# Kernel tuning notes

Measured on AMD Instinct MI355X. Metric: run time of the kernel, lower is better.

## Reference

```python
import jax, jax.numpy as jnp
import numpy as np

N, D, E = 10000, 64, 32768   # nodes, padded degree, target edges
F, H, O = 64, 256, 1         # in_channels, hidden_channels, out_channels


def _linear_init(key, fin, fout):
    kw, kb = jax.random.split(key)
    s = 1.0 / np.sqrt(fin)
    w = jax.random.uniform(kw, (fin, fout), jnp.float32, -s, s)
    b = jax.random.uniform(kb, (fout,), jnp.float32, -s, s)
    return w, b


def setup_inputs() -> dict:
    key = jax.random.key(0)
    ks = jax.random.split(key, 12)
    x = jax.random.normal(ks[0], (N, F), jnp.float32)
    adj_nbr = jax.random.randint(ks[1], (N, D), 0, N)          # padded neighbor lists
    tar_ei = jax.random.randint(ks[2], (2, E), 0, N)           # target edges
    xcn_w1, xcn_b1 = _linear_init(ks[3], F, H)
    xcn_w2, xcn_b2 = _linear_init(ks[4], H, H)
    xcn_w3, xcn_b3 = _linear_init(ks[5], H, H)
    xij_w1, xij_b1 = _linear_init(ks[6], F, H)
    xij_w2, xij_b2 = _linear_init(ks[7], H, H)
    lin_w1, lin_b1 = _linear_init(ks[8], H, H)
    lin_w2, lin_b2 = _linear_init(ks[9], H, O)
    beta = jnp.ones((1,), jnp.float32)
    return dict(x=x, adj_nbr=adj_nbr, tar_ei=tar_ei, beta=beta,
                xcn_w1=xcn_w1, xcn_b1=xcn_b1, xcn_w2=xcn_w2, xcn_b2=xcn_b2,
                xcn_w3=xcn_w3, xcn_b3=xcn_b3,
                xij_w1=xij_w1, xij_b1=xij_b1, xij_w2=xij_w2, xij_b2=xij_b2,
                lin_w1=lin_w1, lin_b1=lin_b1, lin_w2=lin_w2, lin_b2=lin_b2)


def reference(x, adj_nbr, tar_ei, beta,
              xcn_w1, xcn_b1, xcn_w2, xcn_b2, xcn_w3, xcn_b3,
              xij_w1, xij_b1, xij_w2, xij_b2,
              lin_w1, lin_b1, lin_w2, lin_b2):
    relu = jax.nn.relu
    i, j = tar_ei[0], tar_ei[1]
    # adjoverlap: common-neighbor intersection of rows i and j of the adjacency
    ni = adj_nbr[i]                                   # [E, D] neighbors of i
    nj = adj_nbr[j]                                   # [E, D] neighbors of j
    cm = (ni[:, :, None] == nj[:, None, :]).any(-1)   # [E, D] ni[a] in N(j)?
    # spmm_add(cn, x): sum features of common neighbors per target edge
    xcn = jnp.einsum('ed,edf->ef', cm.astype(x.dtype), x[ni])  # [E, F]
    # xijlin(xi * xj): Linear -> ReLU -> Linear
    xij = x[i] * x[j]
    h_ij = relu(xij @ xij_w1 + xij_b1) @ xij_w2 + xij_b2
    # xcnlin(xcn): Linear -> ReLU -> Linear -> ReLU -> Linear
    h_cn = relu(xcn @ xcn_w1 + xcn_b1)
    h_cn = relu(h_cn @ xcn_w2 + xcn_b2)
    h_cn = h_cn @ xcn_w3 + xcn_b3
    # lin(xcnlin(xcn) * beta + xij): Linear -> ReLU -> Linear
    h = relu((h_cn * beta + h_ij) @ lin_w1 + lin_b1)
    return h @ lin_w2 + lin_b2                        # [E, O]
```

## Files before the change

kernel.cpp:

```cpp
#include <hip/hip_runtime.h>

#define NNODES 10000
#define DDEG   64
#define NEDGES 32768
#define FIN    64
#define HID    256

typedef __attribute__((ext_vector_type(8))) __bf16 bf16x8;
typedef __attribute__((ext_vector_type(4))) float  f32x4;

__device__ __forceinline__ unsigned short f2bf(float f) {
    unsigned x = __float_as_uint(f);
    return (unsigned short)((x + 0x7FFFu + ((x >> 16) & 1u)) >> 16);
}
__device__ __forceinline__ float b2f(unsigned short u) {
    return __uint_as_float(((unsigned)u) << 16);
}

#define OFF_XIJ1 0
#define OFF_XIJ2 16384
#define OFF_XCN1 81920
#define OFF_XCN2 98304
#define OFF_XCN3 163840
#define OFF_LIN1 229376
#define WT_TOTAL 294912
#define NTILES   36

__host__ __device__ constexpr int tile_off(int t) {
    return t < 2  ? OFF_XIJ1 + t * 8192
         : t < 10 ? OFF_XIJ2 + (t - 2) * 8192
         : t < 12 ? OFF_XCN1 + (t - 10) * 8192
         : t < 20 ? OFF_XCN2 + (t - 12) * 8192
         : t < 28 ? OFF_XCN3 + (t - 20) * 8192
         :          OFF_LIN1 + (t - 28) * 8192;
}

__device__ __forceinline__ void gll16(const unsigned short* g, unsigned short* l) {
    __builtin_amdgcn_global_load_lds(
        (const __attribute__((address_space(1))) unsigned int*)g,
        (__attribute__((address_space(3))) unsigned int*)l, 16, 0, 0);
}
__device__ __forceinline__ void stage_tile(const unsigned short* g, unsigned short* l,
                                           int tid, int wv) {
#pragma unroll
    for (int c = 0; c < 2; ++c)
        gll16(g + c * 4096 + tid * 8, l + c * 4096 + wv * 512);
}

__global__ __launch_bounds__(256) void edge_prep_k(const float* __restrict__ x,
                                                   const int* __restrict__ adj,
                                                   const int* __restrict__ tar,
                                                   const float* __restrict__ xij_w1,
                                                   const float* __restrict__ xij_w2,
                                                   const float* __restrict__ xcn_w1,
                                                   const float* __restrict__ xcn_w2,
                                                   const float* __restrict__ xcn_w3,
                                                   const float* __restrict__ lin_w1,
                                                   unsigned short* __restrict__ WT,
                                                   unsigned short* __restrict__ xij_g,
                                                   unsigned short* __restrict__ xcn_g) {
    const int wv   = threadIdx.x >> 6;
    const int lane = threadIdx.x & 63;
    const int e    = blockIdx.x * 4 + wv;

    int i = tar[e];
    int j = tar[NEDGES + e];
    int ni = adj[i * DDEG + lane];
    int nj = adj[j * DDEG + lane];
    float xi = x[i * FIN + lane];
    float xj = x[j * FIN + lane];

    bool found = false;
#pragma unroll
    for (int b = 0; b < 64; ++b)
        found |= (ni == (int)__builtin_amdgcn_readlane(nj, b));
    unsigned long long m = __ballot(found);

    float acc = 0.f;
    while (m) {
        int a = __ffsll(m) - 1;
        m &= m - 1;
        int r = (int)__builtin_amdgcn_readlane(ni, a);
        acc += x[r * FIN + lane];
    }
    int sl = lane ^ ((e & 7) << 3);
    xij_g[(size_t)e * FIN + sl] = f2bf(xi * xj);
    xcn_g[(size_t)e * FIN + sl] = f2bf(acc);

    if (blockIdx.x < WT_TOTAL / 256) {
        int idx = blockIdx.x * 256 + threadIdx.x;
        const float* src;
        int r;
        if (idx < OFF_XIJ2)      { r = idx - OFF_XIJ1; src = xij_w1; }
        else if (idx < OFF_XCN1) { r = idx - OFF_XIJ2; src = xij_w2; }
        else if (idx < OFF_XCN2) { r = idx - OFF_XCN1; src = xcn_w1; }
        else if (idx < OFF_XCN3) { r = idx - OFF_XCN2; src = xcn_w2; }
        else if (idx < OFF_LIN1) { r = idx - OFF_XCN3; src = xcn_w3; }
        else                     { r = idx - OFF_LIN1; src = lin_w1; }
        int kb  = r >> 13;
        int n   = (r & 8191) >> 5;
        int klo = r & 31;
        WT[idx] = f2bf(src[(kb * 32 + klo) * HID + n]);
    }
}

template <int T0, int NT, int LDA>
__device__ __forceinline__ void run_phase(const unsigned short* As,
                                          unsigned short* ring,
                                          const unsigned short* __restrict__ WT,
                                          int lr, int lg, int col0, int r0,
                                          int tid, int wv, f32x4 acc[4][4]) {
#pragma unroll
    for (int m = 0; m < 4; ++m)
#pragma unroll
        for (int n = 0; n < 4; ++n) acc[m][n] = (f32x4){0.f, 0.f, 0.f, 0.f};
    const int sw = (lr & 7) << 3;
#pragma unroll
    for (int s = 0; s < NT; ++s) {
        const int t = T0 + s;
        if (t < NTILES - 1)
            asm volatile("s_waitcnt vmcnt(2) lgkmcnt(0)" ::: "memory");
        else
            asm volatile("s_waitcnt vmcnt(0) lgkmcnt(0)" ::: "memory");
        __builtin_amdgcn_s_barrier();
        if (t + 2 < NTILES)
            stage_tile(WT + tile_off(t + 2), ring + ((t + 2) % 3) * 8192, tid, wv);
        const unsigned short* cur = ring + (t % 3) * 8192;
        bf16x8 a[4], b[4];
#pragma unroll
        for (int n = 0; n < 4; ++n)
            b[n] = *reinterpret_cast<const bf16x8*>(&cur[(col0 + n * 16 + lr) * 32 + 8 * lg]);
#pragma unroll
        for (int m = 0; m < 4; ++m)
            a[m] = *reinterpret_cast<const bf16x8*>(
                &As[(r0 + m * 16 + lr) * LDA + ((s * 32 + 8 * lg) ^ sw)]);
        __builtin_amdgcn_s_setprio(1);
#pragma unroll
        for (int m = 0; m < 4; ++m)
#pragma unroll
            for (int n = 0; n < 4; ++n)
                acc[m][n] = __builtin_amdgcn_mfma_f32_16x16x32_bf16(a[m], b[n], acc[m][n], 0, 0, 0);
        __builtin_amdgcn_s_setprio(0);
    }
}

__global__ __launch_bounds__(512, 1) void mlp_k(const unsigned short* __restrict__ xij_g,
                                                const unsigned short* __restrict__ xcn_g,
                                                const unsigned short* __restrict__ WT,
                                                const float* __restrict__ xij_b1,
                                                const float* __restrict__ xij_b2,
                                                const float* __restrict__ xcn_b1,
                                                const float* __restrict__ xcn_b2,
                                                const float* __restrict__ xcn_b3,
                                                const float* __restrict__ lin_b1,
                                                const float* __restrict__ lin_w2,
                                                const float* __restrict__ lin_b2,
                                                const float* __restrict__ beta,
                                                float* __restrict__ out) {
    __shared__ unsigned short sXij[128 * 64];
    __shared__ unsigned short sXcn[128 * 64];
    __shared__ unsigned short sH[128 * 256];
    __shared__ unsigned short sB[3 * 8192];

    const int tid  = threadIdx.x;
    const int wv   = tid >> 6;
    const int lane = tid & 63;
    const int lr   = lane & 15;
    const int lg   = lane >> 4;
    const int r0   = (wv >> 2) * 64;
    const int col0 = (wv & 3) * 64;
    const int row0 = blockIdx.x * 128;

    stage_tile(xij_g + (size_t)row0 * FIN, sXij, tid, wv);
    stage_tile(xcn_g + (size_t)row0 * FIN, sXcn, tid, wv);
    stage_tile(WT + tile_off(0), sB, tid, wv);
    stage_tile(WT + tile_off(1), sB + 8192, tid, wv);
    const float betaf = beta[0];

    f32x4 acc[4][4];
    float bl[4];

    run_phase<0, 2, 64>(sXij, sB, WT, lr, lg, col0, r0, tid, wv, acc);
#pragma unroll
    for (int n = 0; n < 4; ++n) bl[n] = xij_b1[col0 + n * 16 + lr];
#pragma unroll
    for (int m = 0; m < 4; ++m)
#pragma unroll
        for (int n = 0; n < 4; ++n)
#pragma unroll
            for (int i = 0; i < 4; ++i) {
                int row = r0 + m * 16 + 4 * lg + i;
                int col = col0 + n * 16 + lr;
                sH[row * HID + (col ^ ((row & 7) << 3))] = f2bf(fmaxf(acc[m][n][i] + bl[n], 0.f));
            }

    run_phase<2, 8, 256>(sH, sB, WT, lr, lg, col0, r0, tid, wv, acc);
#pragma unroll
    for (int n = 0; n < 4; ++n) bl[n] = xij_b2[col0 + n * 16 + lr];
    unsigned hij_lo[4][4], hij_hi[4][4];
#pragma unroll
    for (int m = 0; m < 4; ++m)
#pragma unroll
        for (int n = 0; n < 4; ++n) {
            hij_lo[m][n] = ((unsigned)f2bf(acc[m][n][1] + bl[n]) << 16) | f2bf(acc[m][n][0] + bl[n]);
            hij_hi[m][n] = ((unsigned)f2bf(acc[m][n][3] + bl[n]) << 16) | f2bf(acc[m][n][2] + bl[n]);
        }

    run_phase<10, 2, 64>(sXcn, sB, WT, lr, lg, col0, r0, tid, wv, acc);
#pragma unroll
    for (int n = 0; n < 4; ++n) bl[n] = xcn_b1[col0 + n * 16 + lr];
#pragma unroll
    for (int m = 0; m < 4; ++m)
#pragma unroll
        for (int n = 0; n < 4; ++n)
#pragma unroll
            for (int i = 0; i < 4; ++i) {
                int row = r0 + m * 16 + 4 * lg + i;
                int col = col0 + n * 16 + lr;
                sH[row * HID + (col ^ ((row & 7) << 3))] = f2bf(fmaxf(acc[m][n][i] + bl[n], 0.f));
            }

    run_phase<12, 8, 256>(sH, sB, WT, lr, lg, col0, r0, tid, wv, acc);
    asm volatile("s_waitcnt lgkmcnt(0)" ::: "memory");
    __builtin_amdgcn_s_barrier();
#pragma unroll
    for (int n = 0; n < 4; ++n) bl[n] = xcn_b2[col0 + n * 16 + lr];
#pragma unroll
    for (int m = 0; m < 4; ++m)
#pragma unroll
        for (int n = 0; n < 4; ++n)
#pragma unroll
            for (int i = 0; i < 4; ++i) {
                int row = r0 + m * 16 + 4 * lg + i;
                int col = col0 + n * 16 + lr;
                sH[row * HID + (col ^ ((row & 7) << 3))] = f2bf(fmaxf(acc[m][n][i] + bl[n], 0.f));
            }

    run_phase<20, 8, 256>(sH, sB, WT, lr, lg, col0, r0, tid, wv, acc);
    asm volatile("s_waitcnt lgkmcnt(0)" ::: "memory");
    __builtin_amdgcn_s_barrier();
#pragma unroll
    for (int n = 0; n < 4; ++n) bl[n] = xcn_b3[col0 + n * 16 + lr];
#pragma unroll
    for (int m = 0; m < 4; ++m)
#pragma unroll
        for (int n = 0; n < 4; ++n) {
            float h0 = b2f((unsigned short)(hij_lo[m][n] & 0xFFFF));
            float h1 = b2f((unsigned short)(hij_lo[m][n] >> 16));
            float h2 = b2f((unsigned short)(hij_hi[m][n] & 0xFFFF));
            float h3 = b2f((unsigned short)(hij_hi[m][n] >> 16));
            float v0 = (acc[m][n][0] + bl[n]) * betaf + h0;
            float v1 = (acc[m][n][1] + bl[n]) * betaf + h1;
            float v2 = (acc[m][n][2] + bl[n]) * betaf + h2;
            float v3 = (acc[m][n][3] + bl[n]) * betaf + h3;
            int rb = r0 + m * 16 + 4 * lg;
            int col = col0 + n * 16 + lr;
            sH[(rb + 0) * HID + (col ^ (((rb + 0) & 7) << 3))] = f2bf(v0);
            sH[(rb + 1) * HID + (col ^ (((rb + 1) & 7) << 3))] = f2bf(v1);
            sH[(rb + 2) * HID + (col ^ (((rb + 2) & 7) << 3))] = f2bf(v2);
            sH[(rb + 3) * HID + (col ^ (((rb + 3) & 7) << 3))] = f2bf(v3);
        }

    run_phase<28, 8, 256>(sH, sB, WT, lr, lg, col0, r0, tid, wv, acc);
#pragma unroll
    for (int n = 0; n < 4; ++n) bl[n] = lin_b1[col0 + n * 16 + lr];
    float w2l[4];
#pragma unroll
    for (int n = 0; n < 4; ++n) w2l[n] = lin_w2[col0 + n * 16 + lr];
    float* sRed = (float*)sXij;
#pragma unroll
    for (int m = 0; m < 4; ++m) {
        float p[4] = {0.f, 0.f, 0.f, 0.f};
#pragma unroll
        for (int n = 0; n < 4; ++n)
#pragma unroll
            for (int i = 0; i < 4; ++i)
                p[i] += fmaxf(acc[m][n][i] + bl[n], 0.f) * w2l[n];
#pragma unroll
        for (int i = 0; i < 4; ++i) {
            float s = p[i];
            s += __shfl_xor(s, 1);
            s += __shfl_xor(s, 2);
            s += __shfl_xor(s, 4);
            s += __shfl_xor(s, 8);
            if (lr == 0) sRed[(wv & 3) * 128 + r0 + m * 16 + 4 * lg + i] = s;
        }
    }
    __syncthreads();
    if (tid < 128)
        out[row0 + tid] = sRed[tid] + sRed[128 + tid] + sRed[256 + tid] + sRed[384 + tid] + lin_b2[0];
}

extern "C" void kernel_launch(void* const* d_in, const int* in_sizes, int n_in,
                              void* d_out, int out_size, void* d_ws, size_t ws_size,
                              hipStream_t stream) {
    const float* x      = (const float*)d_in[0];
    const int*   adj    = (const int*)d_in[1];
    const int*   tar    = (const int*)d_in[2];
    const float* beta   = (const float*)d_in[3];
    const float* xcn_w1 = (const float*)d_in[4];
    const float* xcn_b1 = (const float*)d_in[5];
    const float* xcn_w2 = (const float*)d_in[6];
    const float* xcn_b2 = (const float*)d_in[7];
    const float* xcn_w3 = (const float*)d_in[8];
    const float* xcn_b3 = (const float*)d_in[9];
    const float* xij_w1 = (const float*)d_in[10];
    const float* xij_b1 = (const float*)d_in[11];
    const float* xij_w2 = (const float*)d_in[12];
    const float* xij_b2 = (const float*)d_in[13];
    const float* lin_w1 = (const float*)d_in[14];
    const float* lin_b1 = (const float*)d_in[15];
    const float* lin_w2 = (const float*)d_in[16];
    const float* lin_b2 = (const float*)d_in[17];

    unsigned short* WT    = (unsigned short*)d_ws;
    unsigned short* xij_g = (unsigned short*)((char*)d_ws + 589824);
    unsigned short* xcn_g = (unsigned short*)((char*)d_ws + 4784128);

    edge_prep_k<<<NEDGES / 4, 256, 0, stream>>>(x, adj, tar,
                                                xij_w1, xij_w2, xcn_w1, xcn_w2, xcn_w3, lin_w1,
                                                WT, xij_g, xcn_g);
    mlp_k<<<NEDGES / 128, 512, 0, stream>>>(xij_g, xcn_g, WT,
                                            xij_b1, xij_b2, xcn_b1, xcn_b2, xcn_b3,
                                            lin_b1, lin_w2, lin_b2, beta, (float*)d_out);
}
```

Before: 62.60 us.

## Stage weight tiles in pairs, spill h_ij to global, share one input buffer

```diff
diff --git a/kernel.cpp b/kernel.cpp
--- a/kernel.cpp
+++ b/kernel.cpp
@@ -25,6 +25,7 @@
 #define OFF_LIN1 229376
 #define WT_TOTAL 294912
 #define NTILES   36
+#define NSS_ALL  18
 
 __host__ __device__ constexpr int tile_off(int t) {
     return t < 2  ? OFF_XIJ1 + t * 8192
@@ -45,6 +46,14 @@
 #pragma unroll
     for (int c = 0; c < 2; ++c)
         gll16(g + c * 4096 + tid * 8, l + c * 4096 + wv * 512);
+}
+__device__ __forceinline__ void stage_pair(const unsigned short* __restrict__ WT, int g,
+                                           unsigned short* ring, int tid, int wv) {
+    const unsigned short* src = WT + tile_off(2 * g);
+    unsigned short* dst = ring + ((2 * g) & 3) * 8192;
+#pragma unroll
+    for (int c = 0; c < 4; ++c)
+        gll16(src + c * 4096 + tid * 8, dst + c * 4096 + wv * 512);
 }
 
 __global__ __launch_bounds__(256) void edge_prep_k(const float* __restrict__ x,
@@ -104,10 +113,12 @@
     }
 }
 
-template <int T0, int NT, int LDA>
+template <int G0, int NSS, int LDA>
 __device__ __forceinline__ void run_phase(const unsigned short* As,
                                           unsigned short* ring,
                                           const unsigned short* __restrict__ WT,
+                                          const unsigned short* __restrict__ restage_src,
+                                          unsigned short* sX,
                                           int lr, int lg, int col0, int r0,
                                           int tid, int wv, f32x4 acc[4][4]) {
 #pragma unroll
@@ -116,37 +127,42 @@
         for (int n = 0; n < 4; ++n) acc[m][n] = (f32x4){0.f, 0.f, 0.f, 0.f};
     const int sw = (lr & 7) << 3;
 #pragma unroll
-    for (int s = 0; s < NT; ++s) {
-        const int t = T0 + s;
-        if (t < NTILES - 1)
-            asm volatile("s_waitcnt vmcnt(2) lgkmcnt(0)" ::: "memory");
-        else
-            asm volatile("s_waitcnt vmcnt(0) lgkmcnt(0)" ::: "memory");
+    for (int ss = 0; ss < NSS; ++ss) {
+        const int g = G0 + ss;
+        asm volatile("s_waitcnt vmcnt(0) lgkmcnt(0)" ::: "memory");
         __builtin_amdgcn_s_barrier();
-        if (t + 2 < NTILES)
-            stage_tile(WT + tile_off(t + 2), ring + ((t + 2) % 3) * 8192, tid, wv);
-        const unsigned short* cur = ring + (t % 3) * 8192;
-        bf16x8 a[4], b[4];
-#pragma unroll
-        for (int n = 0; n < 4; ++n)
-            b[n] = *reinterpret_cast<const bf16x8*>(&cur[(col0 + n * 16 + lr) * 32 + 8 * lg]);
-#pragma unroll
-        for (int m = 0; m < 4; ++m)
-            a[m] = *reinterpret_cast<const bf16x8*>(
-                &As[(r0 + m * 16 + lr) * LDA + ((s * 32 + 8 * lg) ^ sw)]);
-        __builtin_amdgcn_s_setprio(1);
-#pragma unroll
-        for (int m = 0; m < 4; ++m)
+        if (g + 1 < NSS_ALL)
+            stage_pair(WT, g + 1, ring, tid, wv);
+        if (restage_src && ss == 0)
+            stage_tile(restage_src, sX, tid, wv);
+#pragma unroll
+        for (int half = 0; half < 2; ++half) {
+            const int t  = 2 * g + half;
+            const int kk = (ss * 2 + half) * 32;
+            const unsigned short* cur = ring + (t & 3) * 8192;
+            bf16x8 a[4], b[4];
 #pragma unroll
             for (int n = 0; n < 4; ++n)
-                acc[m][n] = __builtin_amdgcn_mfma_f32_16x16x32_bf16(a[m], b[n], acc[m][n], 0, 0, 0);
-        __builtin_amdgcn_s_setprio(0);
+                b[n] = *reinterpret_cast<const bf16x8*>(&cur[(col0 + n * 16 + lr) * 32 + 8 * lg]);
+#pragma unroll
+            for (int m = 0; m < 4; ++m)
+                a[m] = *reinterpret_cast<const bf16x8*>(
+                    &As[(r0 + m * 16 + lr) * LDA + ((kk + 8 * lg) ^ sw)]);
+            __builtin_amdgcn_s_setprio(1);
+#pragma unroll
+            for (int m = 0; m < 4; ++m)
+#pragma unroll
+                for (int n = 0; n < 4; ++n)
+                    acc[m][n] = __builtin_amdgcn_mfma_f32_16x16x32_bf16(a[m], b[n], acc[m][n], 0, 0, 0);
+            __builtin_amdgcn_s_setprio(0);
+        }
     }
 }
 
 __global__ __launch_bounds__(512, 1) void mlp_k(const unsigned short* __restrict__ xij_g,
                                                 const unsigned short* __restrict__ xcn_g,
                                                 const unsigned short* __restrict__ WT,
+                                                unsigned* __restrict__ hij_g,
                                                 const float* __restrict__ xij_b1,
                                                 const float* __restrict__ xij_b2,
                                                 const float* __restrict__ xcn_b1,
@@ -157,10 +173,9 @@
                                                 const float* __restrict__ lin_b2,
                                                 const float* __restrict__ beta,
                                                 float* __restrict__ out) {
-    __shared__ unsigned short sXij[128 * 64];
-    __shared__ unsigned short sXcn[128 * 64];
+    __shared__ unsigned short sX[128 * 64];
     __shared__ unsigned short sH[128 * 256];
-    __shared__ unsigned short sB[3 * 8192];
+    __shared__ unsigned short sB[4 * 8192];
 
     const int tid  = threadIdx.x;
     const int wv   = tid >> 6;
@@ -171,16 +186,15 @@
     const int col0 = (wv & 3) * 64;
     const int row0 = blockIdx.x * 128;
 
-    stage_tile(xij_g + (size_t)row0 * FIN, sXij, tid, wv);
-    stage_tile(xcn_g + (size_t)row0 * FIN, sXcn, tid, wv);
-    stage_tile(WT + tile_off(0), sB, tid, wv);
-    stage_tile(WT + tile_off(1), sB + 8192, tid, wv);
+    stage_tile(xij_g + (size_t)row0 * FIN, sX, tid, wv);
+    stage_pair(WT, 0, sB, tid, wv);
     const float betaf = beta[0];
+    unsigned* hbase = hij_g + (size_t)(blockIdx.x * 8 + wv) * 2048 + lane * 2;
 
     f32x4 acc[4][4];
     float bl[4];
 
-    run_phase<0, 2, 64>(sXij, sB, WT, lr, lg, col0, r0, tid, wv, acc);
+    run_phase<0, 1, 64>(sX, sB, WT, nullptr, nullptr, lr, lg, col0, r0, tid, wv, acc);
 #pragma unroll
     for (int n = 0; n < 4; ++n) bl[n] = xij_b1[col0 + n * 16 + lr];
 #pragma unroll
@@ -194,19 +208,20 @@
                 sH[row * HID + (col ^ ((row & 7) << 3))] = f2bf(fmaxf(acc[m][n][i] + bl[n], 0.f));
             }
 
-    run_phase<2, 8, 256>(sH, sB, WT, lr, lg, col0, r0, tid, wv, acc);
+    run_phase<1, 4, 256>(sH, sB, WT, xcn_g + (size_t)row0 * FIN, sX, lr, lg, col0, r0, tid, wv, acc);
 #pragma unroll
     for (int n = 0; n < 4; ++n) bl[n] = xij_b2[col0 + n * 16 + lr];
-    unsigned hij_lo[4][4], hij_hi[4][4];
 #pragma unroll
     for (int m = 0; m < 4; ++m)
 #pragma unroll
         for (int n = 0; n < 4; ++n) {
-            hij_lo[m][n] = ((unsigned)f2bf(acc[m][n][1] + bl[n]) << 16) | f2bf(acc[m][n][0] + bl[n]);
-            hij_hi[m][n] = ((unsigned)f2bf(acc[m][n][3] + bl[n]) << 16) | f2bf(acc[m][n][2] + bl[n]);
+            uint2 v;
+            v.x = ((unsigned)f2bf(acc[m][n][1] + bl[n]) << 16) | f2bf(acc[m][n][0] + bl[n]);
+            v.y = ((unsigned)f2bf(acc[m][n][3] + bl[n]) << 16) | f2bf(acc[m][n][2] + bl[n]);
+            *reinterpret_cast<uint2*>(hbase + (m * 4 + n) * 128) = v;
         }
 
-    run_phase<10, 2, 64>(sXcn, sB, WT, lr, lg, col0, r0, tid, wv, acc);
+    run_phase<5, 1, 64>(sX, sB, WT, nullptr, nullptr, lr, lg, col0, r0, tid, wv, acc);
 #pragma unroll
     for (int n = 0; n < 4; ++n) bl[n] = xcn_b1[col0 + n * 16 + lr];
 #pragma unroll
@@ -220,7 +235,7 @@
                 sH[row * HID + (col ^ ((row & 7) << 3))] = f2bf(fmaxf(acc[m][n][i] + bl[n], 0.f));
             }
 
-    run_phase<12, 8, 256>(sH, sB, WT, lr, lg, col0, r0, tid, wv, acc);
+    run_phase<6, 4, 256>(sH, sB, WT, nullptr, nullptr, lr, lg, col0, r0, tid, wv, acc);
     asm volatile("s_waitcnt lgkmcnt(0)" ::: "memory");
     __builtin_amdgcn_s_barrier();
 #pragma unroll
@@ -236,7 +251,7 @@
                 sH[row * HID + (col ^ ((row & 7) << 3))] = f2bf(fmaxf(acc[m][n][i] + bl[n], 0.f));
             }
 
-    run_phase<20, 8, 256>(sH, sB, WT, lr, lg, col0, r0, tid, wv, acc);
+    run_phase<10, 4, 256>(sH, sB, WT, nullptr, nullptr, lr, lg, col0, r0, tid, wv, acc);
     asm volatile("s_waitcnt lgkmcnt(0)" ::: "memory");
     __builtin_amdgcn_s_barrier();
 #pragma unroll
@@ -245,10 +260,11 @@
     for (int m = 0; m < 4; ++m)
 #pragma unroll
         for (int n = 0; n < 4; ++n) {
-            float h0 = b2f((unsigned short)(hij_lo[m][n] & 0xFFFF));
-            float h1 = b2f((unsigned short)(hij_lo[m][n] >> 16));
-            float h2 = b2f((unsigned short)(hij_hi[m][n] & 0xFFFF));
-            float h3 = b2f((unsigned short)(hij_hi[m][n] >> 16));
+            uint2 v = *reinterpret_cast<const uint2*>(hbase + (m * 4 + n) * 128);
+            float h0 = b2f((unsigned short)(v.x & 0xFFFF));
+            float h1 = b2f((unsigned short)(v.x >> 16));
+            float h2 = b2f((unsigned short)(v.y & 0xFFFF));
+            float h3 = b2f((unsigned short)(v.y >> 16));
             float v0 = (acc[m][n][0] + bl[n]) * betaf + h0;
             float v1 = (acc[m][n][1] + bl[n]) * betaf + h1;
             float v2 = (acc[m][n][2] + bl[n]) * betaf + h2;
@@ -261,13 +277,13 @@
             sH[(rb + 3) * HID + (col ^ (((rb + 3) & 7) << 3))] = f2bf(v3);
         }
 
-    run_phase<28, 8, 256>(sH, sB, WT, lr, lg, col0, r0, tid, wv, acc);
+    run_phase<14, 4, 256>(sH, sB, WT, nullptr, nullptr, lr, lg, col0, r0, tid, wv, acc);
 #pragma unroll
     for (int n = 0; n < 4; ++n) bl[n] = lin_b1[col0 + n * 16 + lr];
     float w2l[4];
 #pragma unroll
     for (int n = 0; n < 4; ++n) w2l[n] = lin_w2[col0 + n * 16 + lr];
-    float* sRed = (float*)sXij;
+    float* sRed = (float*)sX;
 #pragma unroll
     for (int m = 0; m < 4; ++m) {
         float p[4] = {0.f, 0.f, 0.f, 0.f};
@@ -316,11 +332,12 @@
     unsigned short* WT    = (unsigned short*)d_ws;
     unsigned short* xij_g = (unsigned short*)((char*)d_ws + 589824);
     unsigned short* xcn_g = (unsigned short*)((char*)d_ws + 4784128);
+    unsigned*       hij_g = (unsigned*)((char*)d_ws + 8978432);
 
     edge_prep_k<<<NEDGES / 4, 256, 0, stream>>>(x, adj, tar,
                                                 xij_w1, xij_w2, xcn_w1, xcn_w2, xcn_w3, lin_w1,
                                                 WT, xij_g, xcn_g);
-    mlp_k<<<NEDGES / 128, 512, 0, stream>>>(xij_g, xcn_g, WT,
+    mlp_k<<<NEDGES / 128, 512, 0, stream>>>(xij_g, xcn_g, WT, hij_g,
                                             xij_b1, xij_b2, xcn_b1, xcn_b2, xcn_b3,
                                             lin_b1, lin_w2, lin_b2, beta, (float*)d_out);
 }
```

New measurement: 59.25 us. 5.3% less time.

## Shrink MLP blocks to 64 rows and 4 waves, run two blocks per CU

Applied to the files above, without the earlier changes.

```diff
diff --git a/kernel.cpp b/kernel.cpp
--- a/kernel.cpp
+++ b/kernel.cpp
@@ -43,8 +43,14 @@
 __device__ __forceinline__ void stage_tile(const unsigned short* g, unsigned short* l,
                                            int tid, int wv) {
 #pragma unroll
+    for (int c = 0; c < 4; ++c)
+        gll16(g + c * 2048 + tid * 8, l + c * 2048 + wv * 512);
+}
+__device__ __forceinline__ void stage_act(const unsigned short* g, unsigned short* l,
+                                          int tid, int wv) {
+#pragma unroll
     for (int c = 0; c < 2; ++c)
-        gll16(g + c * 4096 + tid * 8, l + c * 4096 + wv * 512);
+        gll16(g + c * 2048 + tid * 8, l + c * 2048 + wv * 512);
 }
 
 __global__ __launch_bounds__(256) void edge_prep_k(const float* __restrict__ x,
@@ -108,7 +114,9 @@
 __device__ __forceinline__ void run_phase(const unsigned short* As,
                                           unsigned short* ring,
                                           const unsigned short* __restrict__ WT,
-                                          int lr, int lg, int col0, int r0,
+                                          const unsigned short* __restrict__ restage_src,
+                                          unsigned short* sX,
+                                          int lr, int lg, int col0,
                                           int tid, int wv, f32x4 acc[4][4]) {
 #pragma unroll
     for (int m = 0; m < 4; ++m)
@@ -118,14 +126,13 @@
 #pragma unroll
     for (int s = 0; s < NT; ++s) {
         const int t = T0 + s;
-        if (t < NTILES - 1)
-            asm volatile("s_waitcnt vmcnt(2) lgkmcnt(0)" ::: "memory");
-        else
-            asm volatile("s_waitcnt vmcnt(0) lgkmcnt(0)" ::: "memory");
+        asm volatile("s_waitcnt vmcnt(0) lgkmcnt(0)" ::: "memory");
         __builtin_amdgcn_s_barrier();
-        if (t + 2 < NTILES)
-            stage_tile(WT + tile_off(t + 2), ring + ((t + 2) % 3) * 8192, tid, wv);
-        const unsigned short* cur = ring + (t % 3) * 8192;
+        if (t + 1 < NTILES)
+            stage_tile(WT + tile_off(t + 1), ring + ((t + 1) & 1) * 8192, tid, wv);
+        if (restage_src && s == 0)
+            stage_act(restage_src, sX, tid, wv);
+        const unsigned short* cur = ring + (t & 1) * 8192;
         bf16x8 a[4], b[4];
 #pragma unroll
         for (int n = 0; n < 4; ++n)
@@ -133,7 +140,7 @@
 #pragma unroll
         for (int m = 0; m < 4; ++m)
             a[m] = *reinterpret_cast<const bf16x8*>(
-                &As[(r0 + m * 16 + lr) * LDA + ((s * 32 + 8 * lg) ^ sw)]);
+                &As[(m * 16 + lr) * LDA + ((s * 32 + 8 * lg) ^ sw)]);
         __builtin_amdgcn_s_setprio(1);
 #pragma unroll
         for (int m = 0; m < 4; ++m)
@@ -144,7 +151,7 @@
     }
 }
 
-__global__ __launch_bounds__(512, 1) void mlp_k(const unsigned short* __restrict__ xij_g,
+__global__ __launch_bounds__(256, 2) void mlp_k(const unsigned short* __restrict__ xij_g,
                                                 const unsigned short* __restrict__ xcn_g,
                                                 const unsigned short* __restrict__ WT,
                                                 const float* __restrict__ xij_b1,
@@ -157,30 +164,26 @@
                                                 const float* __restrict__ lin_b2,
                                                 const float* __restrict__ beta,
                                                 float* __restrict__ out) {
-    __shared__ unsigned short sXij[128 * 64];
-    __shared__ unsigned short sXcn[128 * 64];
-    __shared__ unsigned short sH[128 * 256];
-    __shared__ unsigned short sB[3 * 8192];
+    __shared__ unsigned short sX[64 * 64];
+    __shared__ unsigned short sH[64 * 256];
+    __shared__ unsigned short sB[2 * 8192];
 
     const int tid  = threadIdx.x;
     const int wv   = tid >> 6;
     const int lane = tid & 63;
     const int lr   = lane & 15;
     const int lg   = lane >> 4;
-    const int r0   = (wv >> 2) * 64;
-    const int col0 = (wv & 3) * 64;
-    const int row0 = blockIdx.x * 128;
-
-    stage_tile(xij_g + (size_t)row0 * FIN, sXij, tid, wv);
-    stage_tile(xcn_g + (size_t)row0 * FIN, sXcn, tid, wv);
+    const int col0 = wv * 64;
+    const int row0 = blockIdx.x * 64;
+
+    stage_act(xij_g + (size_t)row0 * FIN, sX, tid, wv);
     stage_tile(WT + tile_off(0), sB, tid, wv);
-    stage_tile(WT + tile_off(1), sB + 8192, tid, wv);
     const float betaf = beta[0];
 
     f32x4 acc[4][4];
     float bl[4];
 
-    run_phase<0, 2, 64>(sXij, sB, WT, lr, lg, col0, r0, tid, wv, acc);
+    run_phase<0, 2, 64>(sX, sB, WT, nullptr, nullptr, lr, lg, col0, tid, wv, acc);
 #pragma unroll
     for (int n = 0; n < 4; ++n) bl[n] = xij_b1[col0 + n * 16 + lr];
 #pragma unroll
@@ -189,12 +192,12 @@
         for (int n = 0; n < 4; ++n)
 #pragma unroll
             for (int i = 0; i < 4; ++i) {
-                int row = r0 + m * 16 + 4 * lg + i;
+                int row = m * 16 + 4 * lg + i;
                 int col = col0 + n * 16 + lr;
                 sH[row * HID + (col ^ ((row & 7) << 3))] = f2bf(fmaxf(acc[m][n][i] + bl[n], 0.f));
             }
 
-    run_phase<2, 8, 256>(sH, sB, WT, lr, lg, col0, r0, tid, wv, acc);
+    run_phase<2, 8, 256>(sH, sB, WT, xcn_g + (size_t)row0 * FIN, sX, lr, lg, col0, tid, wv, acc);
 #pragma unroll
     for (int n = 0; n < 4; ++n) bl[n] = xij_b2[col0 + n * 16 + lr];
     unsigned hij_lo[4][4], hij_hi[4][4];
@@ -206,7 +209,7 @@
             hij_hi[m][n] = ((unsigned)f2bf(acc[m][n][3] + bl[n]) << 16) | f2bf(acc[m][n][2] + bl[n]);
         }
 
-    run_phase<10, 2, 64>(sXcn, sB, WT, lr, lg, col0, r0, tid, wv, acc);
+    run_phase<10, 2, 64>(sX, sB, WT, nullptr, nullptr, lr, lg, col0, tid, wv, acc);
 #pragma unroll
     for (int n = 0; n < 4; ++n) bl[n] = xcn_b1[col0 + n * 16 + lr];
 #pragma unroll
@@ -215,12 +218,12 @@
         for (int n = 0; n < 4; ++n)
 #pragma unroll
             for (int i = 0; i < 4; ++i) {
-                int row = r0 + m * 16 + 4 * lg + i;
+                int row = m * 16 + 4 * lg + i;
                 int col = col0 + n * 16 + lr;
                 sH[row * HID + (col ^ ((row & 7) << 3))] = f2bf(fmaxf(acc[m][n][i] + bl[n], 0.f));
             }
 
-    run_phase<12, 8, 256>(sH, sB, WT, lr, lg, col0, r0, tid, wv, acc);
+    run_phase<12, 8, 256>(sH, sB, WT, nullptr, nullptr, lr, lg, col0, tid, wv, acc);
     asm volatile("s_waitcnt lgkmcnt(0)" ::: "memory");
     __builtin_amdgcn_s_barrier();
 #pragma unroll
@@ -231,12 +234,12 @@
         for (int n = 0; n < 4; ++n)
 #pragma unroll
             for (int i = 0; i < 4; ++i) {
-                int row = r0 + m * 16 + 4 * lg + i;
+                int row = m * 16 + 4 * lg + i;
                 int col = col0 + n * 16 + lr;
                 sH[row * HID + (col ^ ((row & 7) << 3))] = f2bf(fmaxf(acc[m][n][i] + bl[n], 0.f));
             }
 
-    run_phase<20, 8, 256>(sH, sB, WT, lr, lg, col0, r0, tid, wv, acc);
+    run_phase<20, 8, 256>(sH, sB, WT, nullptr, nullptr, lr, lg, col0, tid, wv, acc);
     asm volatile("s_waitcnt lgkmcnt(0)" ::: "memory");
     __builtin_amdgcn_s_barrier();
 #pragma unroll
@@ -253,7 +256,7 @@
             float v1 = (acc[m][n][1] + bl[n]) * betaf + h1;
             float v2 = (acc[m][n][2] + bl[n]) * betaf + h2;
             float v3 = (acc[m][n][3] + bl[n]) * betaf + h3;
-            int rb = r0 + m * 16 + 4 * lg;
+            int rb = m * 16 + 4 * lg;
             int col = col0 + n * 16 + lr;
             sH[(rb + 0) * HID + (col ^ (((rb + 0) & 7) << 3))] = f2bf(v0);
             sH[(rb + 1) * HID + (col ^ (((rb + 1) & 7) << 3))] = f2bf(v1);
@@ -261,13 +264,13 @@
             sH[(rb + 3) * HID + (col ^ (((rb + 3) & 7) << 3))] = f2bf(v3);
         }
 
-    run_phase<28, 8, 256>(sH, sB, WT, lr, lg, col0, r0, tid, wv, acc);
+    run_phase<28, 8, 256>(sH, sB, WT, nullptr, nullptr, lr, lg, col0, tid, wv, acc);
 #pragma unroll
     for (int n = 0; n < 4; ++n) bl[n] = lin_b1[col0 + n * 16 + lr];
     float w2l[4];
 #pragma unroll
     for (int n = 0; n < 4; ++n) w2l[n] = lin_w2[col0 + n * 16 + lr];
-    float* sRed = (float*)sXij;
+    float* sRed = (float*)sX;
 #pragma unroll
     for (int m = 0; m < 4; ++m) {
         float p[4] = {0.f, 0.f, 0.f, 0.f};
@@ -283,12 +286,12 @@
             s += __shfl_xor(s, 2);
             s += __shfl_xor(s, 4);
             s += __shfl_xor(s, 8);
-            if (lr == 0) sRed[(wv & 3) * 128 + r0 + m * 16 + 4 * lg + i] = s;
+            if (lr == 0) sRed[wv * 64 + m * 16 + 4 * lg + i] = s;
         }
     }
     __syncthreads();
-    if (tid < 128)
-        out[row0 + tid] = sRed[tid] + sRed[128 + tid] + sRed[256 + tid] + sRed[384 + tid] + lin_b2[0];
+    if (tid < 64)
+        out[row0 + tid] = sRed[tid] + sRed[64 + tid] + sRed[128 + tid] + sRed[192 + tid] + lin_b2[0];
 }
 
 extern "C" void kernel_launch(void* const* d_in, const int* in_sizes, int n_in,
@@ -320,7 +323,7 @@
     edge_prep_k<<<NEDGES / 4, 256, 0, stream>>>(x, adj, tar,
                                                 xij_w1, xij_w2, xcn_w1, xcn_w2, xcn_w3, lin_w1,
                                                 WT, xij_g, xcn_g);
-    mlp_k<<<NEDGES / 128, 512, 0, stream>>>(xij_g, xcn_g, WT,
-                                            xij_b1, xij_b2, xcn_b1, xcn_b2, xcn_b3,
-                                            lin_b1, lin_w2, lin_b2, beta, (float*)d_out);
-}
+    mlp_k<<<NEDGES / 64, 256, 0, stream>>>(xij_g, xcn_g, WT,
+                                           xij_b1, xij_b2, xcn_b1, xcn_b2, xcn_b3,
+                                           lin_b1, lin_w2, lin_b2, beta, (float*)d_out);
+}
```

Result: slower. 65.45 us (+4.6%).
